# Optimization experiments

Measured on AMD Instinct MI355X. Metric: run time of the kernel, lower is better.

Reference implementation:

```python
import jax, jax.numpy as jnp
import numpy as np

QMAX = 127.0

def _fq(x):
    # symmetric per-tensor int8 fake-quant with straight-through estimator
    s = jax.lax.stop_gradient(jnp.max(jnp.abs(x))) / QMAX + 1e-8
    q = jnp.clip(jnp.round(x / s), -QMAX - 1.0, QMAX) * s
    return x + jax.lax.stop_gradient(q - x)

def _ln(x, g, b):
    m = jnp.mean(x, axis=-1, keepdims=True)
    v = jnp.var(x, axis=-1, keepdims=True)
    return (x - m) * jax.lax.rsqrt(v + 1e-6) * g + b

def setup_inputs() -> dict:
    key = jax.random.key(0)
    ks = jax.random.split(key, 8)
    B, N, C = 64, 197, 768
    Dff = 4 * C
    sd = lambda k, shape, fan: jax.random.normal(k, shape, jnp.float32) * (fan ** -0.5)
    return {
        "x": jax.random.normal(ks[0], (B, N, C), jnp.float32),
        "w_qkv": sd(ks[1], (3 * C, C), C), "b_qkv": jnp.zeros((3 * C,), jnp.float32),
        "w_proj": sd(ks[2], (C, C), C), "b_proj": jnp.zeros((C,), jnp.float32),
        "w_fc1": sd(ks[3], (Dff, C), C), "b_fc1": jnp.zeros((Dff,), jnp.float32),
        "w_fc2": sd(ks[4], (C, Dff), Dff), "b_fc2": jnp.zeros((C,), jnp.float32),
        "g1": jnp.ones((C,), jnp.float32), "be1": jnp.zeros((C,), jnp.float32),
        "g2": jnp.ones((C,), jnp.float32), "be2": jnp.zeros((C,), jnp.float32),
    }

def reference(x, w_qkv, b_qkv, w_proj, b_proj, w_fc1, b_fc1, w_fc2, b_fc2, g1, be1, g2, be2):
    B, N, C = x.shape
    H = 12
    Dh = C // H
    scale = Dh ** -0.5
    # norm1 (QLayerNorm: LN + fake-quant output)
    xn = _fq(_ln(x, g1, be1))
    # attn_qkv (QuantLinear: fake-quant weight) + attn_qkv_output (QAct)
    qkv = _fq(xn @ _fq(w_qkv).T + b_qkv)
    qkv = qkv.reshape(B, N, 3, H, Dh).transpose(2, 0, 3, 1, 4)  # [3,B,H,N,Dh]
    q, k, v = qkv[0], qkv[1], qkv[2]
    attn = jnp.einsum('bhnd,bhmd->bhnm', q, k) * scale
    # intSoft (QuantIntSoft: integer-approx softmax modeled as softmax + fake-quant)
    attn = _fq(jax.nn.softmax(attn, axis=-1))
    xa = jnp.einsum('bhnm,bhmd->bhnd', attn, v).transpose(0, 2, 1, 3).reshape(B, N, C)
    # attn_proj (QuantLinear) + sv_attn (QAct)
    xa = _fq(xa @ _fq(w_proj).T + b_proj)
    # residual1 (QAct)
    x = _fq(x + xa)
    # norm2 + MLP
    xn2 = _fq(_ln(x, g2, be2))
    h = xn2 @ _fq(w_fc1).T + b_fc1
    h = _fq(jax.nn.gelu(h, approximate=False))  # mlp_act (QAct with GELU)
    h = h @ _fq(w_fc2).T + b_fc2
    # residual2 (QAct)
    x = _fq(x + h)
    return x
```

## Files before the change

### kernel.cpp

```cpp
#include <hip/hip_runtime.h>
#include <hip/hip_bf16.h>
#include <math.h>

typedef _Float16 f16_t;
typedef _Float16 f16x8 __attribute__((ext_vector_type(8)));
typedef signed char i8x8 __attribute__((ext_vector_type(8)));
typedef float f32x4 __attribute__((ext_vector_type(4)));

#define MFMA_F16 __builtin_amdgcn_mfma_f32_16x16x32_f16

#define B_      64
#define N_TOK   197
#define C_      768
#define H_      12
#define DH      64
#define DFF     3072
#define M_VALID (B_*N_TOK)
#define M_PAD   12672
#define NP      208
#define NKP     224
#define BH      (B_*H_)
#define PLDS    232

#define S_WQKV 0
#define S_WPROJ 1
#define S_WFC1 2
#define S_WFC2 3
#define S_LN1 4
#define S_QKV 5
#define S_LMIN 6
#define S_PROJ 7
#define S_R1 8
#define S_LN2 9
#define S_GELU 10
#define S_R2 11

#define EPI_AMX   0
#define EPI_CODE8 1
#define EPI_GAMX  2
#define EPI_GCODE8 3
#define EPI_F32   4

__device__ __forceinline__ float wred_max(float v){
  #pragma unroll
  for (int o = 32; o; o >>= 1) v = fmaxf(v, __shfl_xor(v, o));
  return v;
}
__device__ __forceinline__ float wred_min(float v){
  #pragma unroll
  for (int o = 32; o; o >>= 1) v = fminf(v, __shfl_xor(v, o));
  return v;
}
__device__ __forceinline__ float wred_sum(float v){
  #pragma unroll
  for (int o = 32; o; o >>= 1) v += __shfl_xor(v, o);
  return v;
}
__device__ __forceinline__ void atomicMaxPosF(float* p, float v){
  atomicMax((int*)p, __float_as_int(v));
}
__device__ __forceinline__ void block_amax_commit(float m, float* slot){
  __shared__ float smx[4];
  int t = threadIdx.x, wave = t >> 6, lane = t & 63;
  m = wred_max(m);
  if (lane == 0) smx[wave] = m;
  __syncthreads();
  if (t == 0){
    float r = fmaxf(fmaxf(smx[0], smx[1]), fmaxf(smx[2], smx[3]));
    atomicMaxPosF(slot, r);
  }
}
__device__ __forceinline__ float fq_scale(float amax){ return amax / 127.0f + 1e-8f; }
__device__ __forceinline__ float fq_q(float x, float s){
  return fminf(fmaxf(rintf(x / s), -128.0f), 127.0f);
}
__device__ __forceinline__ float fq_apply(float x, float s){ return fq_q(x, s) * s; }
__device__ __forceinline__ float gelu_f(float v){
  return 0.5f * v * (1.0f + erff(v * 0.70710678118654752440f));
}
__device__ __forceinline__ f16x8 cvt_i8_f16(i8x8 v){
  f16x8 r;
  #pragma unroll
  for (int i = 0; i < 8; ++i) r[i] = (_Float16)(short)v[i];
  return r;
}

__global__ void k_init(float* slots){
  int i = threadIdx.x;
  if (i < 32) slots[i] = 0.0f;
  if (i == S_LMIN) ((unsigned int*)slots)[i] = 0x7F800000u;
}

__global__ void k_fill(float* p, long n, float val){
  long i = (long)blockIdx.x * blockDim.x + threadIdx.x;
  long st = (long)gridDim.x * blockDim.x;
  for (; i < n; i += st) p[i] = val;
}

__global__ __launch_bounds__(256) void k_amax(const float* __restrict__ p, long n4, float* slot){
  long i = (long)blockIdx.x * blockDim.x + threadIdx.x;
  long st = (long)gridDim.x * blockDim.x;
  const f32x4* p4 = (const f32x4*)p;
  float m = 0.0f;
  for (; i < n4; i += st){
    f32x4 v = p4[i];
    m = fmaxf(m, fmaxf(fmaxf(fabsf(v[0]), fabsf(v[1])), fmaxf(fabsf(v[2]), fabsf(v[3]))));
  }
  block_amax_commit(m, slot);
}

__global__ void k_wcode(const float* __restrict__ in, f16_t* __restrict__ out,
                        const float* amax, long n){
  float s = fq_scale(*amax);
  long i = (long)blockIdx.x * blockDim.x + threadIdx.x;
  long st = (long)gridDim.x * blockDim.x;
  for (; i < n; i += st) out[i] = (f16_t)fq_q(in[i], s);
}

__global__ __launch_bounds__(256) void k_fq_f32(const float* __restrict__ in,
    float* __restrict__ out, const float* amax, long n4){
  float s = fq_scale(*amax);
  long i = (long)blockIdx.x * blockDim.x + threadIdx.x;
  long st = (long)gridDim.x * blockDim.x;
  const f32x4* in4 = (const f32x4*)in;
  f32x4* out4 = (f32x4*)out;
  for (; i < n4; i += st){
    f32x4 v = in4[i];
    #pragma unroll
    for (int e = 0; e < 4; ++e) v[e] = fq_apply(v[e], s);
    out4[i] = v;
  }
}

template<bool STORE>
__global__ __launch_bounds__(64) void k_ln(const float* __restrict__ x,
    const float* __restrict__ g, const float* __restrict__ b,
    signed char* __restrict__ y8, const float* scale_slot, float* amax_slot){
  int row = blockIdx.x, lane = threadIdx.x;
  const float* xr = x + (long)row * C_;
  float v[12]; float s = 0.0f;
  #pragma unroll
  for (int i = 0; i < 12; ++i){ v[i] = xr[lane + 64*i]; s += v[i]; }
  s = wred_sum(s);
  float mean = s / 768.0f;
  float q = 0.0f;
  #pragma unroll
  for (int i = 0; i < 12; ++i){ float d = v[i] - mean; q += d*d; }
  q = wred_sum(q);
  float inv = rsqrtf(q / 768.0f + 1e-6f);
  if (STORE){
    float fs = fq_scale(*scale_slot);
    signed char* yr = y8 + (long)row * C_;
    #pragma unroll
    for (int i = 0; i < 12; ++i){
      int c = lane + 64*i;
      float o = (v[i] - mean) * inv * g[c] + b[c];
      yr[c] = (signed char)(int)fq_q(o, fs);
    }
  } else {
    float mx = 0.0f;
    #pragma unroll
    for (int i = 0; i < 12; ++i){
      int c = lane + 64*i;
      float o = (v[i] - mean) * inv * g[c] + b[c];
      mx = fmaxf(mx, fabsf(o));
    }
    mx = wred_max(mx);
    if (lane == 0) atomicMaxPosF(amax_slot, mx);
  }
}

template<bool FQRAW>
__global__ __launch_bounds__(256) void k_res(float* __restrict__ raw, const float* amax_raw,
                      const float* __restrict__ xin, float* amax_out, long n4){
  float s = 0.0f;
  if (FQRAW) s = fq_scale(*amax_raw);
  long i = (long)blockIdx.x * blockDim.x + threadIdx.x;
  long st = (long)gridDim.x * blockDim.x;
  f32x4* raw4 = (f32x4*)raw;
  const f32x4* xin4 = (const f32x4*)xin;
  float mx = 0.0f;
  for (; i < n4; i += st){
    f32x4 v = raw4[i];
    f32x4 xv = xin4[i];
    #pragma unroll
    for (int e = 0; e < 4; ++e){
      float t = FQRAW ? fq_apply(v[e], s) : v[e];
      float r = xv[e] + t;
      v[e] = r;
      mx = fmaxf(mx, fabsf(r));
    }
    raw4[i] = v;
  }
  block_amax_commit(mx, amax_out);
}

template<int EPI>
__global__ __launch_bounds__(256) void k_gemm(const signed char* __restrict__ A8,
    const f16_t* __restrict__ W, const float* __restrict__ bias,
    float* __restrict__ Cf, signed char* __restrict__ C8,
    const float* __restrict__ sA, const float* __restrict__ sW,
    const float* __restrict__ sOut, float* __restrict__ amax_slot,
    int Mv, int N, int K){
  __shared__ __align__(16) f16_t As[128*32];
  __shared__ __align__(16) f16_t Ws[128*32];
  const int bm = blockIdx.y * 128, bn = blockIdx.x * 128;
  const int t = threadIdx.x;
  const int lane = t & 63;
  const int wave = t >> 6;
  const int wr = (wave >> 1) * 64, wc = (wave & 1) * 64;
  const int lr = lane & 15, lkb = (lane >> 4) * 8;
  f32x4 acc[4][4] = {};
  for (int k0 = 0; k0 < K; k0 += 32){
    __syncthreads();
    {
      int r = t >> 1, c = (t & 1) << 4;
      long gg = (long)(bm + r)*K + k0 + c;
      i8x8 c0 = *(const i8x8*)&A8[gg];
      i8x8 c1 = *(const i8x8*)&A8[gg + 8];
      *(f16x8*)&As[r*32 + c]     = cvt_i8_f16(c0);
      *(f16x8*)&As[r*32 + c + 8] = cvt_i8_f16(c1);
    }
    #pragma unroll
    for (int n = 0; n < 2; ++n){
      int p = t*8 + n*2048;
      int r = p >> 5, c = p & 31;
      *(f16x8*)&Ws[p] = *(const f16x8*)&W[(long)(bn + r)*K + k0 + c];
    }
    __syncthreads();
    f16x8 af[4], wf[4];
    #pragma unroll
    for (int i = 0; i < 4; ++i){
      af[i] = *(const f16x8*)&As[(wr + i*16 + lr)*32 + lkb];
      wf[i] = *(const f16x8*)&Ws[(wc + i*16 + lr)*32 + lkb];
    }
    #pragma unroll
    for (int mf = 0; mf < 4; ++mf)
      #pragma unroll
      for (int nf = 0; nf < 4; ++nf)
        acc[mf][nf] = MFMA_F16(af[mf], wf[nf], acc[mf][nf], 0, 0, 0);
  }
  const float sc = fq_scale(*sA) * fq_scale(*sW);
  float fs = 0.0f;
  if (EPI == EPI_CODE8 || EPI == EPI_GCODE8) fs = fq_scale(*sOut);
  float mx = 0.0f;
  const int rl = (lane >> 4) * 4;
  #pragma unroll
  for (int mf = 0; mf < 4; ++mf){
    #pragma unroll
    for (int j = 0; j < 4; ++j){
      int row = bm + wr + mf*16 + rl + j;
      bool valid = row < Mv;
      #pragma unroll
      for (int nf = 0; nf < 4; ++nf){
        int col = bn + wc + nf*16 + lr;
        float v = acc[mf][nf][j] * sc + bias[col];
        if (EPI == EPI_GAMX || EPI == EPI_GCODE8) v = gelu_f(v);
        if (EPI == EPI_AMX || EPI == EPI_GAMX){
          if (valid) mx = fmaxf(mx, fabsf(v));
        } else if (EPI == EPI_CODE8){
          if (valid) C8[(long)row*N + col] = (signed char)(int)fq_q(v, fs);
        } else if (EPI == EPI_GCODE8){
          C8[(long)row*N + col] = valid ? (signed char)(int)fq_q(v, fs) : (signed char)0;
        } else if (EPI == EPI_F32){
          if (valid) Cf[(long)row*N + col] = v;
        }
      }
    }
  }
  if (EPI == EPI_AMX || EPI == EPI_GAMX){
    mx = wred_max(mx);
    if (lane == 0) atomicMaxPosF(amax_slot, mx);
  }
}

__global__ __launch_bounds__(256) void k_gemmp(const f16_t* __restrict__ Ahi,
    const f16_t* __restrict__ Alo, const f16_t* __restrict__ W,
    const float* __restrict__ bias, float* __restrict__ Cf,
    const unsigned int* __restrict__ lmin_slot, const float* __restrict__ sQkv,
    const float* __restrict__ sW, float* __restrict__ amax_slot,
    int Mv, int N, int K){
  __shared__ __align__(16) f16_t Ah[128*32];
  __shared__ __align__(16) f16_t Al[128*32];
  __shared__ __align__(16) f16_t Ws[128*32];
  const int bm = blockIdx.y * 128, bn = blockIdx.x * 128;
  const int t = threadIdx.x;
  const int lane = t & 63;
  const int wave = t >> 6;
  const int wr = (wave >> 1) * 64, wc = (wave & 1) * 64;
  const int lr = lane & 15, lkb = (lane >> 4) * 8;
  f32x4 acc[4][4] = {};
  for (int k0 = 0; k0 < K; k0 += 32){
    __syncthreads();
    #pragma unroll
    for (int n = 0; n < 2; ++n){
      int p = t*8 + n*2048;
      int r = p >> 5, c = p & 31;
      *(f16x8*)&Ah[p] = *(const f16x8*)&Ahi[(long)(bm + r)*K + k0 + c];
      *(f16x8*)&Al[p] = *(const f16x8*)&Alo[(long)(bm + r)*K + k0 + c];
      *(f16x8*)&Ws[p] = *(const f16x8*)&W[(long)(bn + r)*K + k0 + c];
    }
    __syncthreads();
    f16x8 ah[4], al[4], wf[4];
    #pragma unroll
    for (int i = 0; i < 4; ++i){
      ah[i] = *(const f16x8*)&Ah[(wr + i*16 + lr)*32 + lkb];
      al[i] = *(const f16x8*)&Al[(wr + i*16 + lr)*32 + lkb];
      wf[i] = *(const f16x8*)&Ws[(wc + i*16 + lr)*32 + lkb];
    }
    #pragma unroll
    for (int mf = 0; mf < 4; ++mf)
      #pragma unroll
      for (int nf = 0; nf < 4; ++nf){
        acc[mf][nf] = MFMA_F16(ah[mf], wf[nf], acc[mf][nf], 0, 0, 0);
        acc[mf][nf] = MFMA_F16(al[mf], wf[nf], acc[mf][nf], 0, 0, 0);
      }
  }
  float sa_p = (1.0f / __uint_as_float(*lmin_slot)) / 127.0f + 1e-8f;
  const float cs = sa_p * fq_scale(*sQkv) * fq_scale(*sW) * 2048.0f;
  float mx = 0.0f;
  const int rl = (lane >> 4) * 4;
  #pragma unroll
  for (int mf = 0; mf < 4; ++mf){
    #pragma unroll
    for (int j = 0; j < 4; ++j){
      int row = bm + wr + mf*16 + rl + j;
      if (row < Mv){
        #pragma unroll
        for (int nf = 0; nf < 4; ++nf){
          int col = bn + wc + nf*16 + lr;
          float v = acc[mf][nf][j] * cs + bias[col];
          Cf[(long)row*N + col] = v;
          mx = fmaxf(mx, fabsf(v));
        }
      }
    }
  }
  mx = wred_max(mx);
  if (lane == 0) atomicMaxPosF(amax_slot, mx);
}

__global__ __launch_bounds__(64) void k_vtrans(const signed char* __restrict__ qkv8,
                                               f16_t* __restrict__ vt){
  int bh = blockIdx.x; int b = bh / H_, h = bh % H_, d = threadIdx.x;
  long coff = 1536 + h*64 + d;
  for (int m8 = 0; m8 < NKP/8; ++m8){
    f16_t vv[8];
    #pragma unroll
    for (int e = 0; e < 8; ++e){
      int m = m8*8 + e;
      signed char code = (m < N_TOK) ? qkv8[(long)(b*N_TOK + m)*2304 + coff] : (signed char)0;
      vv[e] = (f16_t)(short)code;
    }
    *(f16x8*)&vt[((long)bh*DH + d)*NKP + m8*8] = *(f16x8*)vv;
  }
}

__global__ __launch_bounds__(64) void k_attn1(const signed char* __restrict__ qkv8,
    const float* __restrict__ sQkv, float* __restrict__ marr,
    float* __restrict__ larr, unsigned int* lmin_slot){
  int rt = blockIdx.x, bh = blockIdx.y;
  int b = bh / H_, h = bh % H_;
  int lane = threadIdx.x, lr = lane & 15, lkb = (lane >> 4) * 8;
  float sq = fq_scale(*sQkv);
  float s2 = sq * sq * 0.125f;
  int qn = rt*16 + lr; if (qn > N_TOK-1) qn = N_TOK-1;
  long qoff = (long)(b*N_TOK + qn)*2304 + h*64 + lkb;
  f16x8 a0 = cvt_i8_f16(*(const i8x8*)&qkv8[qoff]);
  f16x8 a1 = cvt_i8_f16(*(const i8x8*)&qkv8[qoff + 32]);
  float m[4], l[4];
  #pragma unroll
  for (int j = 0; j < 4; ++j){ m[j] = -1e30f; l[j] = 0.0f; }
  for (int ct = 0; ct < NKP/16; ++ct){
    int kn = ct*16 + lr; int knc = kn > N_TOK-1 ? N_TOK-1 : kn;
    long koff = (long)(b*N_TOK + knc)*2304 + 768 + h*64 + lkb;
    f16x8 b0 = cvt_i8_f16(*(const i8x8*)&qkv8[koff]);
    f16x8 b1 = cvt_i8_f16(*(const i8x8*)&qkv8[koff + 32]);
    f32x4 sacc = {};
    sacc = MFMA_F16(a0, b0, sacc, 0, 0, 0);
    sacc = MFMA_F16(a1, b1, sacc, 0, 0, 0);
    bool cv = kn < N_TOK;
    #pragma unroll
    for (int j = 0; j < 4; ++j){
      float sv = cv ? sacc[j]*s2 : -1e30f;
      float mn = fmaxf(m[j], sv);
      l[j] = l[j]*expf(m[j]-mn) + expf(sv-mn);
      m[j] = mn;
    }
  }
  #pragma unroll
  for (int mask = 1; mask < 16; mask <<= 1){
    #pragma unroll
    for (int j = 0; j < 4; ++j){
      float mo = __shfl_xor(m[j], mask);
      float lo = __shfl_xor(l[j], mask);
      float mn = fmaxf(m[j], mo);
      l[j] = l[j]*expf(m[j]-mn) + lo*expf(mo-mn);
      m[j] = mn;
    }
  }
  float lmn = 3.4e38f;
  #pragma unroll
  for (int j = 0; j < 4; ++j){
    int r = rt*16 + (lane >> 4)*4 + j;
    if (r < N_TOK) lmn = fminf(lmn, l[j]);
    if (lr == 0 && r < NP){ marr[(long)bh*NP + r] = m[j]; larr[(long)bh*NP + r] = l[j]; }
  }
  lmn = wred_min(lmn);
  if (lane == 0) atomicMin(lmin_slot, __float_as_uint(lmn));
}

__global__ __launch_bounds__(64) void k_attn2pv(const signed char* __restrict__ qkv8,
    const f16_t* __restrict__ vt, const float* __restrict__ sQkv,
    const float* __restrict__ marr, const float* __restrict__ larr,
    const unsigned int* lmin_slot, f16_t* __restrict__ xa_hi, f16_t* __restrict__ xa_lo){
  __shared__ __align__(16) f16_t Pl[16*PLDS];
  int rt = blockIdx.x, bh = blockIdx.y;
  int b = bh / H_, h = bh % H_;
  int lane = threadIdx.x, lr = lane & 15, lkb = (lane >> 4) * 8;
  float sq = fq_scale(*sQkv);
  float s2 = sq * sq * 0.125f;
  float lmin = __uint_as_float(*lmin_slot);
  float sa = (1.0f / lmin) / 127.0f + 1e-8f;
  int qn = rt*16 + lr; if (qn > N_TOK-1) qn = N_TOK-1;
  long qoff = (long)(b*N_TOK + qn)*2304 + h*64 + lkb;
  f16x8 a0 = cvt_i8_f16(*(const i8x8*)&qkv8[qoff]);
  f16x8 a1 = cvt_i8_f16(*(const i8x8*)&qkv8[qoff + 32]);
  int rbase = (lane >> 4)*4;
  float pm[4], pinv[4];
  #pragma unroll
  for (int j = 0; j < 4; ++j){
    int r = rt*16 + rbase + j;
    pm[j] = marr[(long)bh*NP + r];
    pinv[j] = 1.0f / larr[(long)bh*NP + r];
  }
  for (int ct = 0; ct < NKP/16; ++ct){
    int kn = ct*16 + lr; int knc = kn > N_TOK-1 ? N_TOK-1 : kn;
    long koff = (long)(b*N_TOK + knc)*2304 + 768 + h*64 + lkb;
    f16x8 b0 = cvt_i8_f16(*(const i8x8*)&qkv8[koff]);
    f16x8 b1 = cvt_i8_f16(*(const i8x8*)&qkv8[koff + 32]);
    f32x4 sacc = {};
    sacc = MFMA_F16(a0, b0, sacc, 0, 0, 0);
    sacc = MFMA_F16(a1, b1, sacc, 0, 0, 0);
    bool cv = kn < N_TOK;
    #pragma unroll
    for (int j = 0; j < 4; ++j){
      int r = rt*16 + rbase + j;
      float p = 0.0f;
      if (cv && r < N_TOK) p = expf(sacc[j]*s2 - pm[j]) * pinv[j];
      float qp = fminf(rintf(p / sa), 127.0f);
      Pl[(rbase + j)*PLDS + ct*16 + lr] = (f16_t)qp;
    }
  }
  __syncthreads();
  f32x4 acc[4] = {};
  for (int k0 = 0; k0 < NKP; k0 += 32){
    f16x8 a = *(const f16x8*)&Pl[lr*PLDS + k0 + lkb];
    #pragma unroll
    for (int nf = 0; nf < 4; ++nf){
      f16x8 bb = *(const f16x8*)&vt[((long)bh*DH + nf*16 + lr)*NKP + k0 + lkb];
      acc[nf] = MFMA_F16(a, bb, acc[nf], 0, 0, 0);
    }
  }
  #pragma unroll
  for (int j = 0; j < 4; ++j){
    int n = rt*16 + rbase + j;
    if (n < N_TOK){
      long orow = (long)(b*N_TOK + n)*C_ + h*DH;
      #pragma unroll
      for (int nf = 0; nf < 4; ++nf){
        float I  = acc[nf][j];
        float hi = rintf(I * (1.0f/2048.0f));
        float lo = (I - hi * 2048.0f) * (1.0f/2048.0f);
        xa_hi[orow + nf*16 + lr] = (f16_t)hi;
        xa_lo[orow + nf*16 + lr] = (f16_t)lo;
      }
    }
  }
}

static inline int cdiv_i(long a, long b){ return (int)((a + b - 1) / b); }

extern "C" void kernel_launch(void* const* d_in, const int* in_sizes, int n_in,
                              void* d_out, int out_size, void* d_ws, size_t ws_size,
                              hipStream_t stream){
  const float* x      = (const float*)d_in[0];
  const float* w_qkv  = (const float*)d_in[1];
  const float* b_qkv  = (const float*)d_in[2];
  const float* w_proj = (const float*)d_in[3];
  const float* b_proj = (const float*)d_in[4];
  const float* w_fc1  = (const float*)d_in[5];
  const float* b_fc1  = (const float*)d_in[6];
  const float* w_fc2  = (const float*)d_in[7];
  const float* b_fc2  = (const float*)d_in[8];
  const float* g1     = (const float*)d_in[9];
  const float* be1    = (const float*)d_in[10];
  const float* g2     = (const float*)d_in[11];
  const float* be2    = (const float*)d_in[12];
  float* out = (float*)d_out;

  char* ws = (char*)d_ws;
  size_t off = 0;
  float* slots  = (float*)ws;              off += 1024;
  f16_t* wqkv_c = (f16_t*)(ws + off);      off += (size_t)2304*768*2;
  f16_t* wproj_c= (f16_t*)(ws + off);      off += (size_t)768*768*2;
  f16_t* wfc1_c = (f16_t*)(ws + off);      off += (size_t)3072*768*2;
  f16_t* wfc2_c = (f16_t*)(ws + off);      off += (size_t)768*3072*2;
  signed char* xn8 = (signed char*)(ws + off); off += (size_t)M_PAD*C_;
  char* r1 = ws + off;
  signed char* qkv8 = (signed char*)r1;
  f16_t* vtb  = (f16_t*)(r1 + (size_t)M_VALID*2304);
  float* marr = (float*)(r1 + (size_t)M_VALID*2304 + (size_t)BH*DH*NKP*2);
  float* larr = marr + (size_t)BH*NP;
  size_t xa_off = (size_t)M_VALID*2304 + (size_t)BH*DH*NKP*2 + 2*(size_t)BH*NP*4;
  f16_t* xa_hi = (f16_t*)(r1 + xa_off);
  f16_t* xa_lo = (f16_t*)(r1 + xa_off + (size_t)M_PAD*C_*2);
  size_t r1_sz = xa_off + 2*(size_t)M_PAD*C_*2;
  float* x1 = (float*)r1;
  signed char* h8 = (signed char*)(r1 + (size_t)M_VALID*C_*4);
  off += r1_sz;
  const size_t NEED = off;

  if (ws_size < NEED){
    k_fill<<<256, 256, 0, stream>>>(out, out_size, 1.0e4f);
    return;
  }

  const long nW1 = (long)2304*768, nW2 = (long)768*768, nW3 = (long)3072*768, nW4 = (long)768*3072;
  const long nXC = (long)M_VALID*C_;
  const long nXC4 = nXC/4;
  float* raw = out;

  k_init<<<1, 64, 0, stream>>>(slots);
  hipMemsetAsync(xn8 + (size_t)M_VALID*C_, 0, (size_t)(M_PAD - M_VALID)*C_, stream);
  hipMemsetAsync(xa_hi + (size_t)M_VALID*C_, 0, (size_t)(M_PAD - M_VALID)*C_*2, stream);
  hipMemsetAsync(xa_lo + (size_t)M_VALID*C_, 0, (size_t)(M_PAD - M_VALID)*C_*2, stream);

  k_amax<<<1024, 256, 0, stream>>>(w_qkv, nW1/4, &slots[S_WQKV]);
  k_amax<<<512, 256, 0, stream>>>(w_proj, nW2/4, &slots[S_WPROJ]);
  k_amax<<<1024, 256, 0, stream>>>(w_fc1, nW3/4, &slots[S_WFC1]);
  k_amax<<<1024, 256, 0, stream>>>(w_fc2, nW4/4, &slots[S_WFC2]);
  k_wcode<<<cdiv_i(nW1,256), 256, 0, stream>>>(w_qkv, wqkv_c, &slots[S_WQKV], nW1);
  k_wcode<<<cdiv_i(nW2,256), 256, 0, stream>>>(w_proj, wproj_c, &slots[S_WPROJ], nW2);
  k_wcode<<<cdiv_i(nW3,256), 256, 0, stream>>>(w_fc1, wfc1_c, &slots[S_WFC1], nW3);
  k_wcode<<<cdiv_i(nW4,256), 256, 0, stream>>>(w_fc2, wfc2_c, &slots[S_WFC2], nW4);

  k_ln<false><<<M_VALID, 64, 0, stream>>>(x, g1, be1, nullptr, nullptr, &slots[S_LN1]);
  k_ln<true ><<<M_VALID, 64, 0, stream>>>(x, g1, be1, xn8, &slots[S_LN1], nullptr);

  k_gemm<EPI_AMX><<<dim3(18, 99), 256, 0, stream>>>(xn8, wqkv_c, b_qkv,
      nullptr, nullptr, &slots[S_LN1], &slots[S_WQKV], nullptr, &slots[S_QKV], M_VALID, 2304, 768);
  k_gemm<EPI_CODE8><<<dim3(18, 99), 256, 0, stream>>>(xn8, wqkv_c, b_qkv,
      nullptr, qkv8, &slots[S_LN1], &slots[S_WQKV], &slots[S_QKV], nullptr, M_VALID, 2304, 768);

  k_vtrans<<<BH, 64, 0, stream>>>(qkv8, vtb);
  k_attn1<<<dim3(NP/16, BH), 64, 0, stream>>>(qkv8, &slots[S_QKV], marr, larr,
      (unsigned int*)&slots[S_LMIN]);
  k_attn2pv<<<dim3(NP/16, BH), 64, 0, stream>>>(qkv8, vtb, &slots[S_QKV], marr, larr,
      (const unsigned int*)&slots[S_LMIN], xa_hi, xa_lo);

  k_gemmp<<<dim3(6, 99), 256, 0, stream>>>(xa_hi, xa_lo, wproj_c, b_proj, raw,
      (const unsigned int*)&slots[S_LMIN], &slots[S_QKV], &slots[S_WPROJ], &slots[S_PROJ],
      M_VALID, 768, 768);
  k_res<true><<<1040, 256, 0, stream>>>(raw, &slots[S_PROJ], x, &slots[S_R1], nXC4);
  k_fq_f32<<<2080, 256, 0, stream>>>(raw, x1, &slots[S_R1], nXC4);

  k_ln<false><<<M_VALID, 64, 0, stream>>>(x1, g2, be2, nullptr, nullptr, &slots[S_LN2]);
  k_ln<true ><<<M_VALID, 64, 0, stream>>>(x1, g2, be2, xn8, &slots[S_LN2], nullptr);

  k_gemm<EPI_GAMX><<<dim3(24, 99), 256, 0, stream>>>(xn8, wfc1_c, b_fc1,
      nullptr, nullptr, &slots[S_LN2], &slots[S_WFC1], nullptr, &slots[S_GELU], M_VALID, 3072, 768);
  k_gemm<EPI_GCODE8><<<dim3(24, 99), 256, 0, stream>>>(xn8, wfc1_c, b_fc1,
      nullptr, h8, &slots[S_LN2], &slots[S_WFC1], &slots[S_GELU], nullptr, M_VALID, 3072, 768);

  k_gemm<EPI_F32><<<dim3(6, 99), 256, 0, stream>>>(h8, wfc2_c, b_fc2,
      raw, nullptr, &slots[S_GELU], &slots[S_WFC2], nullptr, nullptr, M_VALID, 768, 3072);
  k_res<false><<<1040, 256, 0, stream>>>(raw, nullptr, x1, &slots[S_R2], nXC4);
  k_fq_f32<<<2080, 256, 0, stream>>>(raw, out, &slots[S_R2], nXC4);
}
```

Baseline: 1.652 ms.

## Store GEMM activations as fp16 codes, pad LDS rows, compute GELU amax from max

Measured after the change: 1.564 ms. 5.3% less time.

```diff
diff --git a/kernel.cpp b/kernel.cpp
--- a/kernel.cpp
+++ b/kernel.cpp
@@ -21,6 +21,7 @@
 #define NKP     224
 #define BH      (B_*H_)
 #define PLDS    232
+#define LS      40
 
 #define S_WQKV 0
 #define S_WPROJ 1
@@ -35,11 +36,11 @@
 #define S_GELU 10
 #define S_R2 11
 
-#define EPI_AMX   0
-#define EPI_CODE8 1
-#define EPI_GAMX  2
-#define EPI_GCODE8 3
-#define EPI_F32   4
+#define EPI_AMX    0
+#define EPI_CODE8  1
+#define EPI_VMAX   2
+#define EPI_GCODE16 3
+#define EPI_F32    4
 
 __device__ __forceinline__ float wred_max(float v){
   #pragma unroll
@@ -97,6 +98,10 @@
   for (; i < n; i += st) p[i] = val;
 }
 
+__global__ void k_gelu_amax(float* slot){
+  if (threadIdx.x == 0) *slot = fmaxf(gelu_f(*slot), 0.16997120f);
+}
+
 __global__ __launch_bounds__(256) void k_amax(const float* __restrict__ p, long n4, float* slot){
   long i = (long)blockIdx.x * blockDim.x + threadIdx.x;
   long st = (long)gridDim.x * blockDim.x;
@@ -135,7 +140,7 @@
 template<bool STORE>
 __global__ __launch_bounds__(64) void k_ln(const float* __restrict__ x,
     const float* __restrict__ g, const float* __restrict__ b,
-    signed char* __restrict__ y8, const float* scale_slot, float* amax_slot){
+    f16_t* __restrict__ y16, const float* scale_slot, float* amax_slot){
   int row = blockIdx.x, lane = threadIdx.x;
   const float* xr = x + (long)row * C_;
   float v[12]; float s = 0.0f;
@@ -150,12 +155,12 @@
   float inv = rsqrtf(q / 768.0f + 1e-6f);
   if (STORE){
     float fs = fq_scale(*scale_slot);
-    signed char* yr = y8 + (long)row * C_;
+    f16_t* yr = y16 + (long)row * C_;
     #pragma unroll
     for (int i = 0; i < 12; ++i){
       int c = lane + 64*i;
       float o = (v[i] - mean) * inv * g[c] + b[c];
-      yr[c] = (signed char)(int)fq_q(o, fs);
+      yr[c] = (f16_t)fq_q(o, fs);
     }
   } else {
     float mx = 0.0f;
@@ -196,14 +201,14 @@
 }
 
 template<int EPI>
-__global__ __launch_bounds__(256) void k_gemm(const signed char* __restrict__ A8,
+__global__ __launch_bounds__(256) void k_gemm(const f16_t* __restrict__ A16,
     const f16_t* __restrict__ W, const float* __restrict__ bias,
-    float* __restrict__ Cf, signed char* __restrict__ C8,
+    float* __restrict__ Cf, signed char* __restrict__ C8, f16_t* __restrict__ C16,
     const float* __restrict__ sA, const float* __restrict__ sW,
     const float* __restrict__ sOut, float* __restrict__ amax_slot,
     int Mv, int N, int K){
-  __shared__ __align__(16) f16_t As[128*32];
-  __shared__ __align__(16) f16_t Ws[128*32];
+  __shared__ __align__(16) f16_t As[128*LS];
+  __shared__ __align__(16) f16_t Ws[128*LS];
   const int bm = blockIdx.y * 128, bn = blockIdx.x * 128;
   const int t = threadIdx.x;
   const int lane = t & 63;
@@ -213,26 +218,19 @@
   f32x4 acc[4][4] = {};
   for (int k0 = 0; k0 < K; k0 += 32){
     __syncthreads();
-    {
-      int r = t >> 1, c = (t & 1) << 4;
-      long gg = (long)(bm + r)*K + k0 + c;
-      i8x8 c0 = *(const i8x8*)&A8[gg];
-      i8x8 c1 = *(const i8x8*)&A8[gg + 8];
-      *(f16x8*)&As[r*32 + c]     = cvt_i8_f16(c0);
-      *(f16x8*)&As[r*32 + c + 8] = cvt_i8_f16(c1);
-    }
     #pragma unroll
     for (int n = 0; n < 2; ++n){
       int p = t*8 + n*2048;
       int r = p >> 5, c = p & 31;
-      *(f16x8*)&Ws[p] = *(const f16x8*)&W[(long)(bn + r)*K + k0 + c];
+      *(f16x8*)&As[r*LS + c] = *(const f16x8*)&A16[(long)(bm + r)*K + k0 + c];
+      *(f16x8*)&Ws[r*LS + c] = *(const f16x8*)&W[(long)(bn + r)*K + k0 + c];
     }
     __syncthreads();
     f16x8 af[4], wf[4];
     #pragma unroll
     for (int i = 0; i < 4; ++i){
-      af[i] = *(const f16x8*)&As[(wr + i*16 + lr)*32 + lkb];
-      wf[i] = *(const f16x8*)&Ws[(wc + i*16 + lr)*32 + lkb];
+      af[i] = *(const f16x8*)&As[(wr + i*16 + lr)*LS + lkb];
+      wf[i] = *(const f16x8*)&Ws[(wc + i*16 + lr)*LS + lkb];
     }
     #pragma unroll
     for (int mf = 0; mf < 4; ++mf)
@@ -242,7 +240,7 @@
   }
   const float sc = fq_scale(*sA) * fq_scale(*sW);
   float fs = 0.0f;
-  if (EPI == EPI_CODE8 || EPI == EPI_GCODE8) fs = fq_scale(*sOut);
+  if (EPI == EPI_CODE8 || EPI == EPI_GCODE16) fs = fq_scale(*sOut);
   float mx = 0.0f;
   const int rl = (lane >> 4) * 4;
   #pragma unroll
@@ -255,20 +253,22 @@
       for (int nf = 0; nf < 4; ++nf){
         int col = bn + wc + nf*16 + lr;
         float v = acc[mf][nf][j] * sc + bias[col];
-        if (EPI == EPI_GAMX || EPI == EPI_GCODE8) v = gelu_f(v);
-        if (EPI == EPI_AMX || EPI == EPI_GAMX){
+        if (EPI == EPI_AMX){
           if (valid) mx = fmaxf(mx, fabsf(v));
+        } else if (EPI == EPI_VMAX){
+          if (valid) mx = fmaxf(mx, v);
         } else if (EPI == EPI_CODE8){
           if (valid) C8[(long)row*N + col] = (signed char)(int)fq_q(v, fs);
-        } else if (EPI == EPI_GCODE8){
-          C8[(long)row*N + col] = valid ? (signed char)(int)fq_q(v, fs) : (signed char)0;
+        } else if (EPI == EPI_GCODE16){
+          float o = valid ? fq_q(gelu_f(v), fs) : 0.0f;
+          C16[(long)row*N + col] = (f16_t)o;
         } else if (EPI == EPI_F32){
           if (valid) Cf[(long)row*N + col] = v;
         }
       }
     }
   }
-  if (EPI == EPI_AMX || EPI == EPI_GAMX){
+  if (EPI == EPI_AMX || EPI == EPI_VMAX){
     mx = wred_max(mx);
     if (lane == 0) atomicMaxPosF(amax_slot, mx);
   }
@@ -280,9 +280,9 @@
     const unsigned int* __restrict__ lmin_slot, const float* __restrict__ sQkv,
     const float* __restrict__ sW, float* __restrict__ amax_slot,
     int Mv, int N, int K){
-  __shared__ __align__(16) f16_t Ah[128*32];
-  __shared__ __align__(16) f16_t Al[128*32];
-  __shared__ __align__(16) f16_t Ws[128*32];
+  __shared__ __align__(16) f16_t Ah[128*LS];
+  __shared__ __align__(16) f16_t Al[128*LS];
+  __shared__ __align__(16) f16_t Ws[128*LS];
   const int bm = blockIdx.y * 128, bn = blockIdx.x * 128;
   const int t = threadIdx.x;
   const int lane = t & 63;
@@ -296,17 +296,17 @@
     for (int n = 0; n < 2; ++n){
       int p = t*8 + n*2048;
       int r = p >> 5, c = p & 31;
-      *(f16x8*)&Ah[p] = *(const f16x8*)&Ahi[(long)(bm + r)*K + k0 + c];
-      *(f16x8*)&Al[p] = *(const f16x8*)&Alo[(long)(bm + r)*K + k0 + c];
-      *(f16x8*)&Ws[p] = *(const f16x8*)&W[(long)(bn + r)*K + k0 + c];
+      *(f16x8*)&Ah[r*LS + c] = *(const f16x8*)&Ahi[(long)(bm + r)*K + k0 + c];
+      *(f16x8*)&Al[r*LS + c] = *(const f16x8*)&Alo[(long)(bm + r)*K + k0 + c];
+      *(f16x8*)&Ws[r*LS + c] = *(const f16x8*)&W[(long)(bn + r)*K + k0 + c];
     }
     __syncthreads();
     f16x8 ah[4], al[4], wf[4];
     #pragma unroll
     for (int i = 0; i < 4; ++i){
-      ah[i] = *(const f16x8*)&Ah[(wr + i*16 + lr)*32 + lkb];
-      al[i] = *(const f16x8*)&Al[(wr + i*16 + lr)*32 + lkb];
-      wf[i] = *(const f16x8*)&Ws[(wc + i*16 + lr)*32 + lkb];
+      ah[i] = *(const f16x8*)&Ah[(wr + i*16 + lr)*LS + lkb];
+      al[i] = *(const f16x8*)&Al[(wr + i*16 + lr)*LS + lkb];
+      wf[i] = *(const f16x8*)&Ws[(wc + i*16 + lr)*LS + lkb];
     }
     #pragma unroll
     for (int mf = 0; mf < 4; ++mf)
@@ -506,7 +506,7 @@
   f16_t* wproj_c= (f16_t*)(ws + off);      off += (size_t)768*768*2;
   f16_t* wfc1_c = (f16_t*)(ws + off);      off += (size_t)3072*768*2;
   f16_t* wfc2_c = (f16_t*)(ws + off);      off += (size_t)768*3072*2;
-  signed char* xn8 = (signed char*)(ws + off); off += (size_t)M_PAD*C_;
+  f16_t* xn16   = (f16_t*)(ws + off);      off += (size_t)M_PAD*C_*2;
   char* r1 = ws + off;
   signed char* qkv8 = (signed char*)r1;
   f16_t* vtb  = (f16_t*)(r1 + (size_t)M_VALID*2304);
@@ -515,10 +515,11 @@
   size_t xa_off = (size_t)M_VALID*2304 + (size_t)BH*DH*NKP*2 + 2*(size_t)BH*NP*4;
   f16_t* xa_hi = (f16_t*)(r1 + xa_off);
   f16_t* xa_lo = (f16_t*)(r1 + xa_off + (size_t)M_PAD*C_*2);
-  size_t r1_sz = xa_off + 2*(size_t)M_PAD*C_*2;
+  size_t attn_sz = xa_off + 2*(size_t)M_PAD*C_*2;
   float* x1 = (float*)r1;
-  signed char* h8 = (signed char*)(r1 + (size_t)M_VALID*C_*4);
-  off += r1_sz;
+  f16_t* h16 = (f16_t*)(r1 + (size_t)M_VALID*C_*4);
+  size_t mlp_sz = (size_t)M_VALID*C_*4 + (size_t)M_PAD*DFF*2;
+  off += (attn_sz > mlp_sz ? attn_sz : mlp_sz);
   const size_t NEED = off;
 
   if (ws_size < NEED){
@@ -532,7 +533,7 @@
   float* raw = out;
 
   k_init<<<1, 64, 0, stream>>>(slots);
-  hipMemsetAsync(xn8 + (size_t)M_VALID*C_, 0, (size_t)(M_PAD - M_VALID)*C_, stream);
+  hipMemsetAsync(xn16 + (size_t)M_VALID*C_, 0, (size_t)(M_PAD - M_VALID)*C_*2, stream);
   hipMemsetAsync(xa_hi + (size_t)M_VALID*C_, 0, (size_t)(M_PAD - M_VALID)*C_*2, stream);
   hipMemsetAsync(xa_lo + (size_t)M_VALID*C_, 0, (size_t)(M_PAD - M_VALID)*C_*2, stream);
 
@@ -546,12 +547,12 @@
   k_wcode<<<cdiv_i(nW4,256), 256, 0, stream>>>(w_fc2, wfc2_c, &slots[S_WFC2], nW4);
 
   k_ln<false><<<M_VALID, 64, 0, stream>>>(x, g1, be1, nullptr, nullptr, &slots[S_LN1]);
-  k_ln<true ><<<M_VALID, 64, 0, stream>>>(x, g1, be1, xn8, &slots[S_LN1], nullptr);
-
-  k_gemm<EPI_AMX><<<dim3(18, 99), 256, 0, stream>>>(xn8, wqkv_c, b_qkv,
-      nullptr, nullptr, &slots[S_LN1], &slots[S_WQKV], nullptr, &slots[S_QKV], M_VALID, 2304, 768);
-  k_gemm<EPI_CODE8><<<dim3(18, 99), 256, 0, stream>>>(xn8, wqkv_c, b_qkv,
-      nullptr, qkv8, &slots[S_LN1], &slots[S_WQKV], &slots[S_QKV], nullptr, M_VALID, 2304, 768);
+  k_ln<true ><<<M_VALID, 64, 0, stream>>>(x, g1, be1, xn16, &slots[S_LN1], nullptr);
+
+  k_gemm<EPI_AMX><<<dim3(18, 99), 256, 0, stream>>>(xn16, wqkv_c, b_qkv,
+      nullptr, nullptr, nullptr, &slots[S_LN1], &slots[S_WQKV], nullptr, &slots[S_QKV], M_VALID, 2304, 768);
+  k_gemm<EPI_CODE8><<<dim3(18, 99), 256, 0, stream>>>(xn16, wqkv_c, b_qkv,
+      nullptr, qkv8, nullptr, &slots[S_LN1], &slots[S_WQKV], &slots[S_QKV], nullptr, M_VALID, 2304, 768);
 
   k_vtrans<<<BH, 64, 0, stream>>>(qkv8, vtb);
   k_attn1<<<dim3(NP/16, BH), 64, 0, stream>>>(qkv8, &slots[S_QKV], marr, larr,
@@ -566,15 +567,16 @@
   k_fq_f32<<<2080, 256, 0, stream>>>(raw, x1, &slots[S_R1], nXC4);
 
   k_ln<false><<<M_VALID, 64, 0, stream>>>(x1, g2, be2, nullptr, nullptr, &slots[S_LN2]);
-  k_ln<true ><<<M_VALID, 64, 0, stream>>>(x1, g2, be2, xn8, &slots[S_LN2], nullptr);
-
-  k_gemm<EPI_GAMX><<<dim3(24, 99), 256, 0, stream>>>(xn8, wfc1_c, b_fc1,
-      nullptr, nullptr, &slots[S_LN2], &slots[S_WFC1], nullptr, &slots[S_GELU], M_VALID, 3072, 768);
-  k_gemm<EPI_GCODE8><<<dim3(24, 99), 256, 0, stream>>>(xn8, wfc1_c, b_fc1,
-      nullptr, h8, &slots[S_LN2], &slots[S_WFC1], &slots[S_GELU], nullptr, M_VALID, 3072, 768);
-
-  k_gemm<EPI_F32><<<dim3(6, 99), 256, 0, stream>>>(h8, wfc2_c, b_fc2,
-      raw, nullptr, &slots[S_GELU], &slots[S_WFC2], nullptr, nullptr, M_VALID, 768, 3072);
+  k_ln<true ><<<M_VALID, 64, 0, stream>>>(x1, g2, be2, xn16, &slots[S_LN2], nullptr);
+
+  k_gemm<EPI_VMAX><<<dim3(24, 99), 256, 0, stream>>>(xn16, wfc1_c, b_fc1,
+      nullptr, nullptr, nullptr, &slots[S_LN2], &slots[S_WFC1], nullptr, &slots[S_GELU], M_VALID, 3072, 768);
+  k_gelu_amax<<<1, 1, 0, stream>>>(&slots[S_GELU]);
+  k_gemm<EPI_GCODE16><<<dim3(24, 99), 256, 0, stream>>>(xn16, wfc1_c, b_fc1,
+      nullptr, nullptr, h16, &slots[S_LN2], &slots[S_WFC1], &slots[S_GELU], nullptr, M_VALID, 3072, 768);
+
+  k_gemm<EPI_F32><<<dim3(6, 99), 256, 0, stream>>>(h16, wfc2_c, b_fc2,
+      raw, nullptr, nullptr, &slots[S_GELU], &slots[S_WFC2], nullptr, nullptr, M_VALID, 768, 3072);
   k_res<false><<<1040, 256, 0, stream>>>(raw, nullptr, x1, &slots[S_R2], nXC4);
   k_fq_f32<<<2080, 256, 0, stream>>>(raw, out, &slots[S_R2], nXC4);
 }
```
